# Performance work log

Hardware: AMD Instinct MI355X
Metric: run time of the kernel (lower is better)

Reference implementation:

```python
import jax, jax.numpy as jnp
import numpy as np

B, T, H = 2000000, 1, 1
SPIN, TRAINLEN = 1000, 800000
ML, SL = 2.9086, 1.898  # hard-coded moments in the original forward


def setup_inputs() -> dict:
    key = jax.random.key(0)
    ks = jax.random.split(key, 8)
    return {
        "x": jax.random.uniform(ks[0], (B, T, 2), dtype=jnp.float32),
        "y_obs": jax.random.uniform(ks[1], (B, 1), dtype=jnp.float32),
        "weight_r_yom": jax.random.uniform(ks[2], (H, H), dtype=jnp.float32),
        "weight_r_ylm": jax.random.uniform(ks[3], (H, H), dtype=jnp.float32),
        "weight_r_yfm": jax.random.uniform(ks[4], (H, H), dtype=jnp.float32),
        "bias_b0_ylm": jax.random.uniform(ks[5], (H,), dtype=jnp.float32),
        "weight_b2_ylm": jax.random.uniform(ks[6], (H, H), dtype=jnp.float32),
        "theltaC": jax.random.uniform(ks[7], (H, H), dtype=jnp.float32),
        "epoch": 1,
        "time_lag": 0,
    }


def _forward(x, y_obs, weight_r_yom, weight_r_ylm, weight_r_yfm,
             bias_b0_ylm, weight_b2_ylm, theltaC, time_lag):
    Bn, Tn, _ = x.shape
    Hn = weight_r_yom.shape[0]
    N = Bn * Tn  # flattened (b-major, t-minor) step order matches the double loop

    eo = jnp.exp(weight_r_yom); el = jnp.exp(weight_r_ylm); ef = jnp.exp(weight_r_yfm)
    den = eo + el + ef
    oo = (eo / den).reshape(Hn)      # constant output gate (softmax over 3 weights)
    ol1 = (el / den).reshape(Hn)
    expT = jnp.exp(theltaC).reshape(Hn)

    u1 = jnp.broadcast_to(x[..., 0].reshape(N, 1), (N, Hn))
    u2 = x[..., 1].reshape(N, 1)
    # ol3 = addmm(bias, (u2-ml)/sl, W) ; ol = ol1*sigmoid(ol3) : input-driven, precompute
    ol3 = bias_b0_ylm[None, :] + ((u2 - ML) / SL) @ weight_b2_ylm  # (N,H)
    ol = ol1 * jax.nn.sigmoid(ol3)
    f = 1.0 - oo - ol
    valid = (jnp.arange(N) // Tn) >= time_lag  # steps with b < time_lag are skipped

    def step(c, inp):
        u1_i, ol_i, f_i, v = inp
        px = jax.nn.relu(u1_i + c - expT)  # scale_factor = 1
        safe = jnp.where(u1_i == 0.0, 1.0, u1_i)
        ib = jnp.where(u1_i == 0.0, 0.0, px / safe)  # relu(0)=0 branch
        bp = ib * u1_i
        h = oo * c + bp            # h_0 + bp_0
        l = ol_i * c
        c1 = f_i * c + (1.0 - ib) * u1_i
        vf = v.astype(c.dtype)
        outs = (h * vf, c * vf, l * vf, bp * vf, ib * vf, oo * vf, ol_i * vf, f_i * vf)
        return jnp.where(v, c1, c), outs

    c0 = jnp.zeros((Hn,), x.dtype)
    _, (h_n, c_n, l_n, bp_n, g_ib, g_oo, g_ol, g_f) = jax.lax.scan(
        step, c0, (u1, ol, f, valid))

    last = lambda a: a.reshape(Bn, Tn, Hn)[:, -1]  # original overwrites per t, keeps last
    h_n, c_n, l_n, bp_n, g_ib, g_oo, g_ol, g_f = map(
        last, (h_n, c_n, l_n, bp_n, g_ib, g_oo, g_ol, g_f))

    obsstd = jnp.std(y_obs[SPIN:TRAINLEN], ddof=1)  # torch.std is unbiased
    vb = (jnp.arange(Bn) >= time_lag)[:, None]
    obs_std = jnp.where(vb, obsstd, 0.0) * jnp.ones((Bn, Hn), x.dtype)
    h_nout = jnp.concatenate([h_n, obs_std], axis=1)
    return h_n, c_n, l_n, bp_n, g_ib, g_oo, g_ol, g_f, h_nout, obs_std


def reference(x, y_obs, weight_r_yom, weight_r_ylm, weight_r_yfm,
              bias_b0_ylm, weight_b2_ylm, theltaC, epoch, time_lag):
    # epoch is unused by the original forward
    return _forward(x, y_obs, weight_r_yom, weight_r_ylm, weight_r_yfm,
                    bias_b0_ylm, weight_b2_ylm, theltaC, time_lag)
```

## Files before the change

### kernel.cpp

```cpp
#include <hip/hip_runtime.h>
#include <math.h>

namespace {

constexpr int   kSpin      = 1000;
constexpr int   kTrainLen  = 800000;
constexpr float kML        = 2.9086f;
constexpr float kSL        = 1.898f;
constexpr int   kChunk     = 4;
constexpr int   kWarm      = 64;
constexpr int   kRedBlocks = 256;

struct __align__(16) Params {
  float oo, ol1, expT, fcon, w, bias, obsstd, pad;
};

__global__ void reduce_std_kernel(const float* __restrict__ y, int ylen,
                                  double* __restrict__ partials) {
  int n = kTrainLen - kSpin;
  if (ylen < kTrainLen) n = (ylen > kSpin) ? (ylen - kSpin) : 0;
  double s = 0.0, s2 = 0.0;
  for (int i = blockIdx.x * blockDim.x + threadIdx.x; i < n;
       i += gridDim.x * blockDim.x) {
    double v = (double)y[kSpin + i];
    s += v;
    s2 += v * v;
  }
  for (int off = 32; off > 0; off >>= 1) {
    s  += __shfl_down(s, off);
    s2 += __shfl_down(s2, off);
  }
  __shared__ double ls[8], ls2[8];
  const int wid = threadIdx.x >> 6;
  if ((threadIdx.x & 63) == 0) { ls[wid] = s; ls2[wid] = s2; }
  __syncthreads();
  if (threadIdx.x == 0) {
    double ts = 0.0, ts2 = 0.0;
    const int nw = blockDim.x >> 6;
    for (int w = 0; w < nw; ++w) { ts += ls[w]; ts2 += ls2[w]; }
    partials[2 * blockIdx.x]     = ts;
    partials[2 * blockIdx.x + 1] = ts2;
  }
}

__global__ void params_kernel(const float* __restrict__ wyom,
                              const float* __restrict__ wylm,
                              const float* __restrict__ wyfm,
                              const float* __restrict__ b0,
                              const float* __restrict__ wb2,
                              const float* __restrict__ thc,
                              const double* __restrict__ partials,
                              Params* __restrict__ p) {
  if (blockIdx.x != 0 || threadIdx.x != 0) return;
  double s = 0.0, s2 = 0.0;
  for (int i = 0; i < kRedBlocks; ++i) {
    s  += partials[2 * i];
    s2 += partials[2 * i + 1];
  }
  const double n = (double)(kTrainLen - kSpin);
  double var = (s2 - s * s / n) / (n - 1.0);
  if (var < 0.0) var = 0.0;
  const float obsstd = (float)sqrt(var);

  const float eo = expf(wyom[0]), el = expf(wylm[0]), ef = expf(wyfm[0]);
  const float den = eo + el + ef;
  Params q;
  q.oo     = eo / den;
  q.ol1    = el / den;
  q.expT   = expf(thc[0]);
  q.fcon   = 1.0f - q.oo;
  q.w      = wb2[0];
  q.bias   = b0[0];
  q.obsstd = obsstd;
  q.pad    = 0.0f;
  *p = q;
}

__global__ __launch_bounds__(256) void scan_kernel(
    const float4* __restrict__ xq,
    float* __restrict__ out,
    const Params* __restrict__ pp,
    const int* __restrict__ tlp, int N) {
  const int nch = (N + kChunk - 1) / kChunk;
  const int t = blockIdx.x * blockDim.x + threadIdx.x;
  if (t >= nch) return;

  const Params p = *pp;
  const int tl = *tlp;
  const float invSL = 1.0f / kSL;
  const int start = t * kChunk;

  float* __restrict__ out_h  = out;
  float* __restrict__ out_c  = out + 1 * (size_t)N;
  float* __restrict__ out_l  = out + 2 * (size_t)N;
  float* __restrict__ out_bp = out + 3 * (size_t)N;
  float* __restrict__ out_ib = out + 4 * (size_t)N;
  float* __restrict__ out_oo = out + 5 * (size_t)N;
  float* __restrict__ out_ol = out + 6 * (size_t)N;
  float* __restrict__ out_f  = out + 7 * (size_t)N;
  float* __restrict__ out_hn = out + 8 * (size_t)N;
  float* __restrict__ out_os = out + 10 * (size_t)N;

  float c = 0.0f;
  {
    int j0 = start - kWarm;
    if (j0 < tl) j0 = tl;
    const int jb = (j0 & ~1);
#pragma unroll 4
    for (int j = jb; j < start; j += 2) {
      const float4 q = xq[j >> 1];
      if (j >= j0) {
        const float z   = p.bias + ((q.y - kML) * invSL) * p.w;
        const float sig = 1.0f / (1.0f + __expf(-z));
        const float f   = p.fcon - p.ol1 * sig;
        const float px  = fmaxf((q.x + c) - p.expT, 0.0f);
        const float bpc = (q.x != 0.0f) ? px : 0.0f;
        c = f * c + q.x - bpc;
      }
      {
        const float z   = p.bias + ((q.w - kML) * invSL) * p.w;
        const float sig = 1.0f / (1.0f + __expf(-z));
        const float f   = p.fcon - p.ol1 * sig;
        const float px  = fmaxf((q.z + c) - p.expT, 0.0f);
        const float bpc = (q.z != 0.0f) ? px : 0.0f;
        c = f * c + q.z - bpc;
      }
    }
  }

  if (start + kChunk <= N) {
    const float4 qa = xq[(start >> 1) + 0];
    const float4 qb = xq[(start >> 1) + 1];
    const float u1a[4] = {qa.x, qa.z, qb.x, qb.z};
    const float u2a[4] = {qa.y, qa.w, qb.y, qb.w};
    float hv[4], cv[4], lv[4], bpv[4], ibv[4], oov[4], olv[4], fv[4], osv[4];
#pragma unroll
    for (int k = 0; k < 4; ++k) {
      const int i = start + k;
      const float u1 = u1a[k], u2 = u2a[k];
      const float z   = p.bias + ((u2 - kML) * invSL) * p.w;
      const float sig = 1.0f / (1.0f + expf(-z));
      const float ol  = p.ol1 * sig;
      const float f   = p.fcon - ol;
      const float px  = fmaxf((u1 + c) - p.expT, 0.0f);
      const float ib  = (u1 != 0.0f) ? (px / u1) : 0.0f;
      const float bp  = ib * u1;
      const float h   = p.oo * c + bp;
      const float l   = ol * c;
      const float c1  = f * c + (1.0f - ib) * u1;
      const bool  v   = (i >= tl);
      hv[k]  = v ? h  : 0.0f;
      cv[k]  = v ? c  : 0.0f;
      lv[k]  = v ? l  : 0.0f;
      bpv[k] = v ? bp : 0.0f;
      ibv[k] = v ? ib : 0.0f;
      oov[k] = v ? p.oo : 0.0f;
      olv[k] = v ? ol : 0.0f;
      fv[k]  = v ? f  : 0.0f;
      osv[k] = v ? p.obsstd : 0.0f;
      if (v) c = c1;
    }
    *reinterpret_cast<float4*>(out_h  + start) = make_float4(hv[0],  hv[1],  hv[2],  hv[3]);
    *reinterpret_cast<float4*>(out_c  + start) = make_float4(cv[0],  cv[1],  cv[2],  cv[3]);
    *reinterpret_cast<float4*>(out_l  + start) = make_float4(lv[0],  lv[1],  lv[2],  lv[3]);
    *reinterpret_cast<float4*>(out_bp + start) = make_float4(bpv[0], bpv[1], bpv[2], bpv[3]);
    *reinterpret_cast<float4*>(out_ib + start) = make_float4(ibv[0], ibv[1], ibv[2], ibv[3]);
    *reinterpret_cast<float4*>(out_oo + start) = make_float4(oov[0], oov[1], oov[2], oov[3]);
    *reinterpret_cast<float4*>(out_ol + start) = make_float4(olv[0], olv[1], olv[2], olv[3]);
    *reinterpret_cast<float4*>(out_f  + start) = make_float4(fv[0],  fv[1],  fv[2],  fv[3]);
    *reinterpret_cast<float4*>(out_os + start) = make_float4(osv[0], osv[1], osv[2], osv[3]);
    float4* hn = reinterpret_cast<float4*>(out_hn + 2 * (size_t)start);
    hn[0] = make_float4(hv[0], osv[0], hv[1], osv[1]);
    hn[1] = make_float4(hv[2], osv[2], hv[3], osv[3]);
  } else {
    const float2* x2 = reinterpret_cast<const float2*>(xq);
    for (int i = start; i < N; ++i) {
      const float2 xv = x2[i];
      const float u1 = xv.x, u2 = xv.y;
      const float z   = p.bias + ((u2 - kML) * invSL) * p.w;
      const float sig = 1.0f / (1.0f + expf(-z));
      const float ol  = p.ol1 * sig;
      const float f   = p.fcon - ol;
      const float px  = fmaxf((u1 + c) - p.expT, 0.0f);
      const float ib  = (u1 != 0.0f) ? (px / u1) : 0.0f;
      const float bp  = ib * u1;
      const float h   = p.oo * c + bp;
      const float l   = ol * c;
      const float c1  = f * c + (1.0f - ib) * u1;
      const bool  v   = (i >= tl);
      out_h[i]  = v ? h  : 0.0f;
      out_c[i]  = v ? c  : 0.0f;
      out_l[i]  = v ? l  : 0.0f;
      out_bp[i] = v ? bp : 0.0f;
      out_ib[i] = v ? ib : 0.0f;
      out_oo[i] = v ? p.oo : 0.0f;
      out_ol[i] = v ? ol : 0.0f;
      out_f[i]  = v ? f  : 0.0f;
      out_os[i] = v ? p.obsstd : 0.0f;
      out_hn[2 * (size_t)i]     = v ? h : 0.0f;
      out_hn[2 * (size_t)i + 1] = v ? p.obsstd : 0.0f;
      if (v) c = c1;
    }
  }
}

}

extern "C" void kernel_launch(void* const* d_in, const int* in_sizes, int n_in,
                              void* d_out, int out_size, void* d_ws, size_t ws_size,
                              hipStream_t stream) {
  const float* x    = (const float*)d_in[0];
  const float* y    = (const float*)d_in[1];
  const float* wyom = (const float*)d_in[2];
  const float* wylm = (const float*)d_in[3];
  const float* wyfm = (const float*)d_in[4];
  const float* b0   = (const float*)d_in[5];
  const float* wb2  = (const float*)d_in[6];
  const float* thc  = (const float*)d_in[7];
  const int* tlp    = (const int*)d_in[9];

  const int N    = in_sizes[0] / 2;
  const int ylen = in_sizes[1];
  float* out = (float*)d_out;

  double* partials = (double*)d_ws;
  Params* params   = (Params*)((char*)d_ws + 2 * kRedBlocks * sizeof(double));

  reduce_std_kernel<<<kRedBlocks, 256, 0, stream>>>(y, ylen, partials);
  params_kernel<<<1, 64, 0, stream>>>(wyom, wylm, wyfm, b0, wb2, thc,
                                      partials, params);

  const int nch = (N + kChunk - 1) / kChunk;
  scan_kernel<<<(nch + 255) / 256, 256, 0, stream>>>(
      (const float4*)x, out, params, tlp, N);
}
```

Before: 152.8 us.

## Fuse std reduction with params via last-block atomic, vectorize and hoist scan loads

```diff
diff --git a/kernel.cpp b/kernel.cpp
--- a/kernel.cpp
+++ b/kernel.cpp
@@ -15,16 +15,35 @@
   float oo, ol1, expT, fcon, w, bias, obsstd, pad;
 };
 
-__global__ void reduce_std_kernel(const float* __restrict__ y, int ylen,
-                                  double* __restrict__ partials) {
+__device__ __forceinline__ float wstep(float c, float u1, float u2,
+                                       const Params& p, float invSL) {
+  const float z   = p.bias + ((u2 - kML) * invSL) * p.w;
+  const float sig = 1.0f / (1.0f + __expf(-z));
+  const float f   = p.fcon - p.ol1 * sig;
+  const float px  = fmaxf((u1 + c) - p.expT, 0.0f);
+  const float bpc = (u1 != 0.0f) ? px : 0.0f;
+  return f * c + u1 - bpc;
+}
+
+__global__ __launch_bounds__(256) void reduce_params_kernel(
+    const float* __restrict__ y, int ylen,
+    const float* __restrict__ wyom, const float* __restrict__ wylm,
+    const float* __restrict__ wyfm, const float* __restrict__ b0,
+    const float* __restrict__ wb2,  const float* __restrict__ thc,
+    double* __restrict__ partials, unsigned int* __restrict__ counter,
+    Params* __restrict__ p) {
   int n = kTrainLen - kSpin;
   if (ylen < kTrainLen) n = (ylen > kSpin) ? (ylen - kSpin) : 0;
+  const int nv = n >> 2;
+  const float4* __restrict__ y4 = reinterpret_cast<const float4*>(y + kSpin);
+
   double s = 0.0, s2 = 0.0;
-  for (int i = blockIdx.x * blockDim.x + threadIdx.x; i < n;
+  for (int i = blockIdx.x * blockDim.x + threadIdx.x; i < nv;
        i += gridDim.x * blockDim.x) {
-    double v = (double)y[kSpin + i];
-    s += v;
-    s2 += v * v;
+    const float4 v = y4[i];
+    const double a = v.x, b = v.y, cc = v.z, d = v.w;
+    s  += (a + b) + (cc + d);
+    s2 += (a * a + b * b) + (cc * cc + d * d);
   }
   for (int off = 32; off > 0; off >>= 1) {
     s  += __shfl_down(s, off);
@@ -34,33 +53,30 @@
   const int wid = threadIdx.x >> 6;
   if ((threadIdx.x & 63) == 0) { ls[wid] = s; ls2[wid] = s2; }
   __syncthreads();
-  if (threadIdx.x == 0) {
-    double ts = 0.0, ts2 = 0.0;
-    const int nw = blockDim.x >> 6;
-    for (int w = 0; w < nw; ++w) { ts += ls[w]; ts2 += ls2[w]; }
-    partials[2 * blockIdx.x]     = ts;
-    partials[2 * blockIdx.x + 1] = ts2;
-  }
-}
-
-__global__ void params_kernel(const float* __restrict__ wyom,
-                              const float* __restrict__ wylm,
-                              const float* __restrict__ wyfm,
-                              const float* __restrict__ b0,
-                              const float* __restrict__ wb2,
-                              const float* __restrict__ thc,
-                              const double* __restrict__ partials,
-                              Params* __restrict__ p) {
-  if (blockIdx.x != 0 || threadIdx.x != 0) return;
-  double s = 0.0, s2 = 0.0;
-  for (int i = 0; i < kRedBlocks; ++i) {
-    s  += partials[2 * i];
-    s2 += partials[2 * i + 1];
-  }
-  const double n = (double)(kTrainLen - kSpin);
-  double var = (s2 - s * s / n) / (n - 1.0);
+  if (threadIdx.x != 0) return;
+
+  double ts = 0.0, ts2 = 0.0;
+  const int nw = blockDim.x >> 6;
+  for (int w = 0; w < nw; ++w) { ts += ls[w]; ts2 += ls2[w]; }
+  partials[2 * blockIdx.x]     = ts;
+  partials[2 * blockIdx.x + 1] = ts2;
+
+  __threadfence();
+  const unsigned int ticket = atomicAdd(counter, 1u);
+  if (ticket != (unsigned int)(gridDim.x - 1)) return;
+
+  double fs = 0.0, fs2 = 0.0;
+  for (int i = 0; i < (int)gridDim.x; ++i) {
+    fs  += partials[2 * i];
+    fs2 += partials[2 * i + 1];
+  }
+  for (int i = (nv << 2); i < n; ++i) {
+    const double v = y[kSpin + i];
+    fs += v; fs2 += v * v;
+  }
+  const double dn = (double)n;
+  double var = (fs2 - fs * fs / dn) / (dn - 1.0);
   if (var < 0.0) var = 0.0;
-  const float obsstd = (float)sqrt(var);
 
   const float eo = expf(wyom[0]), el = expf(wylm[0]), ef = expf(wyfm[0]);
   const float den = eo + el + ef;
@@ -71,12 +87,12 @@
   q.fcon   = 1.0f - q.oo;
   q.w      = wb2[0];
   q.bias   = b0[0];
-  q.obsstd = obsstd;
+  q.obsstd = (float)sqrt(var);
   q.pad    = 0.0f;
   *p = q;
 }
 
-__global__ __launch_bounds__(256) void scan_kernel(
+__global__ __launch_bounds__(256, 8) void scan_kernel(
     const float4* __restrict__ xq,
     float* __restrict__ out,
     const Params* __restrict__ pp,
@@ -89,6 +105,7 @@
   const int tl = *tlp;
   const float invSL = 1.0f / kSL;
   const int start = t * kChunk;
+  const bool full = (start + kChunk <= N);
 
   float* __restrict__ out_h  = out;
   float* __restrict__ out_c  = out + 1 * (size_t)N;
@@ -101,36 +118,33 @@
   float* __restrict__ out_hn = out + 8 * (size_t)N;
   float* __restrict__ out_os = out + 10 * (size_t)N;
 
+  float4 qa = make_float4(0.f, 0.f, 0.f, 0.f);
+  float4 qb = qa;
+  if (full) {
+    qa = xq[(start >> 1) + 0];
+    qb = xq[(start >> 1) + 1];
+  }
+
   float c = 0.0f;
-  {
+  if (start >= kWarm + tl) {
+    const float4* __restrict__ wq = xq + ((start - kWarm) >> 1);
+#pragma unroll 4
+    for (int it = 0; it < kWarm / 2; ++it) {
+      const float4 q = wq[it];
+      c = wstep(c, q.x, q.y, p, invSL);
+      c = wstep(c, q.z, q.w, p, invSL);
+    }
+  } else {
     int j0 = start - kWarm;
     if (j0 < tl) j0 = tl;
-    const int jb = (j0 & ~1);
-#pragma unroll 4
-    for (int j = jb; j < start; j += 2) {
+    for (int j = (j0 & ~1); j < start; j += 2) {
       const float4 q = xq[j >> 1];
-      if (j >= j0) {
-        const float z   = p.bias + ((q.y - kML) * invSL) * p.w;
-        const float sig = 1.0f / (1.0f + __expf(-z));
-        const float f   = p.fcon - p.ol1 * sig;
-        const float px  = fmaxf((q.x + c) - p.expT, 0.0f);
-        const float bpc = (q.x != 0.0f) ? px : 0.0f;
-        c = f * c + q.x - bpc;
-      }
-      {
-        const float z   = p.bias + ((q.w - kML) * invSL) * p.w;
-        const float sig = 1.0f / (1.0f + __expf(-z));
-        const float f   = p.fcon - p.ol1 * sig;
-        const float px  = fmaxf((q.z + c) - p.expT, 0.0f);
-        const float bpc = (q.z != 0.0f) ? px : 0.0f;
-        c = f * c + q.z - bpc;
-      }
-    }
-  }
-
-  if (start + kChunk <= N) {
-    const float4 qa = xq[(start >> 1) + 0];
-    const float4 qb = xq[(start >> 1) + 1];
+      if (j >= j0) c = wstep(c, q.x, q.y, p, invSL);
+      c = wstep(c, q.z, q.w, p, invSL);
+    }
+  }
+
+  if (full) {
     const float u1a[4] = {qa.x, qa.z, qb.x, qb.z};
     const float u2a[4] = {qa.y, qa.w, qb.y, qb.w};
     float hv[4], cv[4], lv[4], bpv[4], ibv[4], oov[4], olv[4], fv[4], osv[4];
@@ -223,12 +237,13 @@
   const int ylen = in_sizes[1];
   float* out = (float*)d_out;
 
-  double* partials = (double*)d_ws;
-  Params* params   = (Params*)((char*)d_ws + 2 * kRedBlocks * sizeof(double));
-
-  reduce_std_kernel<<<kRedBlocks, 256, 0, stream>>>(y, ylen, partials);
-  params_kernel<<<1, 64, 0, stream>>>(wyom, wylm, wyfm, b0, wb2, thc,
-                                      partials, params);
+  double*       partials = (double*)d_ws;
+  unsigned int* counter  = (unsigned int*)((char*)d_ws + 2 * kRedBlocks * sizeof(double));
+  Params*       params   = (Params*)((char*)d_ws + 2 * kRedBlocks * sizeof(double) + 16);
+
+  hipMemsetAsync(counter, 0, sizeof(unsigned int), stream);
+  reduce_params_kernel<<<kRedBlocks, 256, 0, stream>>>(
+      y, ylen, wyom, wylm, wyfm, b0, wb2, thc, partials, counter, params);
 
   const int nch = (N + kChunk - 1) / kChunk;
   scan_kernel<<<(nch + 255) / 256, 256, 0, stream>>>(
```

Measured after the change: 171.2 us. 1.12x slower.
